# Kernel optimization log

Measured on AMD Instinct MI355X. Metric: run time of the kernel, lower is better.

## Reference

```python
import jax, jax.numpy as jnp
import numpy as np

GAMMA = 0.96875


def setup_inputs() -> dict:
    key = jax.random.key(0)
    kx, kq, kk, kv = jax.random.split(key, 4)
    B, T, D = 4, 2048, 1024
    x = jax.random.normal(kx, (B, T, D), dtype=jnp.float32)
    Wq = jax.random.normal(kq, (D, D), dtype=jnp.float32) * (1.0 / np.sqrt(D))
    Wk = jax.random.normal(kk, (D, D), dtype=jnp.float32) * (1.0 / np.sqrt(D))
    Wv = jax.random.normal(kv, (D, D), dtype=jnp.float32) * (1.0 / np.sqrt(D))
    return {"x": x, "Wq": Wq, "Wk": Wk, "Wv": Wv}


def reference(x, Wq, Wk, Wv):
    # x: [B, T, D_in]; projections are bias-free Dense layers
    B, T, _ = x.shape
    D = Wq.shape[1]
    Q = jnp.einsum("bti,id->btd", x, Wq)  # [B,T,D]
    K = jnp.einsum("bti,id->btd", x, Wk)
    V = jnp.einsum("bti,id->btd", x, Wv)

    gamma = jnp.asarray(GAMMA, x.dtype)

    # Original: s[t] = gamma*s[t-1] + K[:,t,:]^T @ V[:,t,:]   (a [D,D] state,
    # batch is CONTRACTED by the matmul), then only reduce_sum over the last
    # state axis is used. The recurrence is linear, so it collapses exactly to
    # a [D]-vector recurrence with m_t[d] = sum_b K[b,t,d] * (sum_e V[b,t,e]).
    m = jnp.einsum("btd,bt->td", K, V.sum(axis=-1))  # [T,D]

    def step(s, mt):
        s_new = gamma * s + mt
        return s_new, s_new

    # loop runs t = 1..T-1 starting from s = 0; afterwards s[0] = s[1]
    _, states = jax.lax.scan(step, jnp.zeros((D,), x.dtype), m[1:])  # [T-1,D]
    S = jnp.concatenate([states[:1], states], axis=0)  # [T,D]

    # tf.reshape([T,D] -> [-1, T]) is a row-major element scramble, then transpose
    S = S.reshape(-1, T).T  # [T,D] (scrambled, faithful to the original)

    return S[None, :, :] * Q  # broadcast over batch -> [B,T,D]
```

## Files before the change

kernel.cpp:

```cpp
#include <hip/hip_runtime.h>
#include <hip/hip_bf16.h>
#include <cstddef>

#define T_DIM 2048
#define D_DIM 1024
#define GAMMA_F 0.96875f

typedef __attribute__((ext_vector_type(8))) short bf16x8;
typedef __attribute__((ext_vector_type(8))) ushort ushortx8;
typedef __attribute__((ext_vector_type(4))) float f32x4;

#define AS1 __attribute__((address_space(1)))
#define AS3 __attribute__((address_space(3)))

static __device__ inline ushort f2bs(float f) {
    __hip_bfloat16 h = __float2bfloat16(f);
    return *reinterpret_cast<ushort*>(&h);
}

template <int N>
static __device__ __forceinline__ void vm_wait() {
    if constexpr (N == 0)      asm volatile("s_waitcnt vmcnt(0)" ::: "memory");
    else if constexpr (N == 4) asm volatile("s_waitcnt vmcnt(4)" ::: "memory");
    else if constexpr (N == 8) asm volatile("s_waitcnt vmcnt(8)" ::: "memory");
    else                       static_assert(N == 0 || N == 4 || N == 8, "vmcnt");
}
static __device__ __forceinline__ void raw_barrier() {
    asm volatile("s_barrier" ::: "memory");
}

__global__ __launch_bounds__(256) void k_prep(const float* __restrict__ Wk,
                                              const float* __restrict__ Wq,
                                              const float* __restrict__ Wv,
                                              ushort* __restrict__ WTk,
                                              ushort* __restrict__ WTq,
                                              float* __restrict__ wv_sum) {
    const int tid = threadIdx.x;
    if (blockIdx.z == 2) {
        __shared__ float red[4];
        const int i = blockIdx.y * 32 + blockIdx.x;
        const float* row = Wv + (size_t)i * D_DIM;
        float p = 0.f;
        for (int c = tid; c < D_DIM; c += 256) p += row[c];
        for (int o = 32; o; o >>= 1) p += __shfl_down(p, o);
        if ((tid & 63) == 0) red[tid >> 6] = p;
        __syncthreads();
        if (tid == 0) wv_sum[i] = red[0] + red[1] + red[2] + red[3];
        return;
    }
    const float* W = (blockIdx.z == 0) ? Wk : Wq;
    ushort* WT     = (blockIdx.z == 0) ? WTk : WTq;
    __shared__ float tile[32][33];
    const int tx = tid & 31, ty = tid >> 5;
    const int kb = blockIdx.x * 32, nb = blockIdx.y * 32;
    #pragma unroll
    for (int r = 0; r < 4; ++r)
        tile[ty + 8 * r][tx] = W[(size_t)(kb + ty + 8 * r) * 1024 + nb + tx];
    __syncthreads();
    #pragma unroll
    for (int r = 0; r < 4; ++r)
        WT[(size_t)(nb + ty + 8 * r) * 1024 + kb + tx] =
            f2bs(tile[tx][ty + 8 * r]);
}

__global__ __launch_bounds__(256) void k_vsum_y(const float* __restrict__ x,
                                                const float* __restrict__ wv_sum,
                                                ushort* __restrict__ yb,
                                                ushort* __restrict__ xb) {
    __shared__ float xs[4][D_DIM];
    __shared__ float red[4][4];
    const int t = blockIdx.x;
    const int tid = threadIdx.x;
    const int lane = tid & 63, wv = tid >> 6;

    #pragma unroll
    for (int b = 0; b < 4; ++b) {
        const float4* xr = (const float4*)(x + ((size_t)b * T_DIM + t) * D_DIM);
        *(float4*)&xs[b][tid * 4] = xr[tid];
    }
    __syncthreads();

    #pragma unroll
    for (int b = 0; b < 4; ++b) {
        float p = 0.f;
        for (int c = tid; c < D_DIM; c += 256) p += xs[b][c] * wv_sum[c];
        for (int o = 32; o; o >>= 1) p += __shfl_down(p, o);
        if (lane == 0) red[wv][b] = p;
    }
    __syncthreads();

    float vs[4];
    #pragma unroll
    for (int b = 0; b < 4; ++b)
        vs[b] = red[0][b] + red[1][b] + red[2][b] + red[3][b];

    if (tid < 128) {
        const int i0 = tid * 8;
        ushortx8 yv;
        #pragma unroll
        for (int j = 0; j < 8; ++j) {
            float a = 0.f;
            #pragma unroll
            for (int b = 0; b < 4; ++b) a += xs[b][i0 + j] * vs[b];
            yv[j] = f2bs(a);
        }
        *(ushortx8*)(yb + (size_t)t * D_DIM + i0) = yv;
    }
    for (int g = tid; g < 512; g += 256) {
        const int b = g >> 7, i0 = (g & 127) * 8;
        ushortx8 xv;
        #pragma unroll
        for (int j = 0; j < 8; ++j) xv[j] = f2bs(xs[b][i0 + j]);
        *(ushortx8*)(xb + ((size_t)b * T_DIM + t) * D_DIM + i0) = xv;
    }
}

template <int MF, int NF, int EPI>
__global__ __launch_bounds__(256) void k_gemm(const ushort* __restrict__ A,
                                              const ushort* __restrict__ BT,
                                              float* __restrict__ C,
                                              const float* __restrict__ S) {
    constexpr int BM = MF * 32;
    constexpr int BN = NF * 32;
    constexpr int LOADS = BM / 32 + BN / 32;
    __shared__ ushort As[2][BM][64];
    __shared__ ushort Bs[2][BN][64];
    const int tid = threadIdx.x;
    const int lane = tid & 63, wid = tid >> 6;
    const int wr = wid >> 1, wc = wid & 1;
    const int rowBase = blockIdx.x * BM;
    const int colBase = blockIdx.y * BN;

    f32x4 acc[MF][NF];
    #pragma unroll
    for (int i = 0; i < MF; ++i)
        #pragma unroll
        for (int j = 0; j < NF; ++j) acc[i][j] = f32x4{0.f, 0.f, 0.f, 0.f};

    auto stage = [&](int buf, int kb) {
        #pragma unroll
        for (int q = 0; q < BM / 32; ++q) {
            const int s = q * 4096 + tid * 16;
            const int r = s >> 7, grp = (s >> 4) & 7;
            const int gcol = kb + (((grp ^ (r & 7)) & 7) << 3);
            __builtin_amdgcn_global_load_lds(
                (const AS1 void*)(A + (size_t)(rowBase + r) * 1024 + gcol),
                (AS3 void*)((AS3 char*)&As[buf][0][0] + s), 16, 0, 0);
        }
        #pragma unroll
        for (int q = 0; q < BN / 32; ++q) {
            const int s = q * 4096 + tid * 16;
            const int r = s >> 7, grp = (s >> 4) & 7;
            const int gcol = kb + (((grp ^ (r & 7)) & 7) << 3);
            __builtin_amdgcn_global_load_lds(
                (const AS1 void*)(BT + (size_t)(colBase + r) * 1024 + gcol),
                (AS3 void*)((AS3 char*)&Bs[buf][0][0] + s), 16, 0, 0);
        }
    };

    stage(0, 0);

    #pragma unroll 2
    for (int kt = 0; kt < 16; ++kt) {
        const int cur = kt & 1;
        if (kt < 15) {
            stage(cur ^ 1, (kt + 1) * 64);
            vm_wait<LOADS>();
        } else {
            vm_wait<0>();
        }
        raw_barrier();

        bf16x8 af[2][MF], bfv[2][NF];
        #pragma unroll
        for (int ks = 0; ks < 2; ++ks) {
            const int kg = ks * 4 + (lane >> 4);
            #pragma unroll
            for (int mi = 0; mi < MF; ++mi) {
                const int r = wr * (MF * 16) + mi * 16 + (lane & 15);
                af[ks][mi] = *(const bf16x8*)((const char*)&As[cur][0][0] +
                                              r * 128 + (((kg ^ (r & 7)) & 7) << 4));
            }
            #pragma unroll
            for (int ni = 0; ni < NF; ++ni) {
                const int r = wc * (NF * 16) + ni * 16 + (lane & 15);
                bfv[ks][ni] = *(const bf16x8*)((const char*)&Bs[cur][0][0] +
                                               r * 128 + (((kg ^ (r & 7)) & 7) << 4));
            }
        }
        #pragma unroll
        for (int ks = 0; ks < 2; ++ks)
            #pragma unroll
            for (int mi = 0; mi < MF; ++mi)
                #pragma unroll
                for (int ni = 0; ni < NF; ++ni)
                    acc[mi][ni] = __builtin_amdgcn_mfma_f32_16x16x32_bf16(
                        af[ks][mi], bfv[ks][ni], acc[mi][ni], 0, 0, 0);

        asm volatile("s_waitcnt lgkmcnt(0)" ::: "memory");
        raw_barrier();
    }

    #pragma unroll
    for (int mi = 0; mi < MF; ++mi) {
        #pragma unroll
        for (int ni = 0; ni < NF; ++ni) {
            const int col = colBase + wc * (NF * 16) + ni * 16 + (lane & 15);
            #pragma unroll
            for (int q = 0; q < 4; ++q) {
                const int row = rowBase + wr * (MF * 16) + mi * 16 + (lane >> 4) * 4 + q;
                float v = acc[mi][ni][q];
                if (EPI) {
                    const int t = row & (T_DIM - 1);
                    v *= S[(size_t)(2 * col + (t >> 10)) * D_DIM + (t & 1023)];
                }
                C[(size_t)row * D_DIM + col] = v;
            }
        }
    }
}

#define SC_L 32
#define SC_NC 64

__global__ __launch_bounds__(256) void k_scan1(const float* __restrict__ m,
                                               float* __restrict__ tot) {
    const int col = blockIdx.x * 64 + (threadIdx.x & 63);
    const int ch  = blockIdx.y * 4 + (threadIdx.x >> 6);
    const int t0 = ch * SC_L;
    float r = 0.f;
    #pragma unroll 4
    for (int k = 0; k < SC_L; ++k) {
        const int t = t0 + k;
        const float a = (t == 0) ? 0.f : m[(size_t)t * D_DIM + col];
        r = GAMMA_F * r + a;
    }
    tot[(size_t)ch * D_DIM + col] = r;
}

__global__ __launch_bounds__(256) void k_scan2(float* __restrict__ m,
                                               const float* __restrict__ tot) {
    const int col = blockIdx.x * 64 + (threadIdx.x & 63);
    const int ch  = blockIdx.y * 4 + (threadIdx.x >> 6);
    const int t0 = ch * SC_L;

    float gL = 1.f;
    #pragma unroll
    for (int i = 0; i < SC_L; ++i) gL *= GAMMA_F;

    float carry = 0.f, f = 1.f;
    for (int j = ch - 1; j >= 0; --j) {
        carry += f * tot[(size_t)j * D_DIM + col];
        f *= gL;
    }

    float r = carry, s1 = 0.f;
    #pragma unroll 4
    for (int k = 0; k < SC_L; ++k) {
        const int t = t0 + k;
        const float a = (t == 0) ? 0.f : m[(size_t)t * D_DIM + col];
        r = GAMMA_F * r + a;
        m[(size_t)t * D_DIM + col] = r;
        if (t == 1) s1 = r;
    }
    if (ch == 0) m[col] = s1;
}

extern "C" void kernel_launch(void* const* d_in, const int* in_sizes, int n_in,
                              void* d_out, int out_size, void* d_ws, size_t ws_size,
                              hipStream_t stream) {
    const float* x  = (const float*)d_in[0];
    const float* Wq = (const float*)d_in[1];
    const float* Wk = (const float*)d_in[2];
    const float* Wv = (const float*)d_in[3];
    float* out = (float*)d_out;
    char* ws = (char*)d_ws;

    ushort* xb  = (ushort*)(ws);
    float*  m   = (float*)(ws + (16u << 20));
    ushort* yb  = (ushort*)(ws + (24u << 20));
    ushort* WTk = (ushort*)(ws + (28u << 20));
    ushort* WTq = (ushort*)(ws + (30u << 20));
    float*  wv_sum = m;
    float*  tot = (float*)yb;

    dim3 gP(32, 32, 3);
    k_prep<<<gP, 256, 0, stream>>>(Wk, Wq, Wv, WTk, WTq, wv_sum);

    k_vsum_y<<<T_DIM, 256, 0, stream>>>(x, wv_sum, (ushort*)yb, (ushort*)xb);

    dim3 gm(T_DIM / 64, D_DIM / 64);
    k_gemm<2, 2, 0><<<gm, 256, 0, stream>>>(yb, WTk, m, nullptr);

    dim3 gs(D_DIM / 64, SC_NC / 4);
    k_scan1<<<gs, 256, 0, stream>>>(m, tot);
    k_scan2<<<gs, 256, 0, stream>>>(m, tot);

    dim3 gq((4 * T_DIM) / 128, D_DIM / 128);
    k_gemm<4, 4, 1><<<gq, 256, 0, stream>>>(xb, WTq, out, m);
}
```

Before: 90.08 us.

## Pre-scramble scan state into GEMM-friendly layout and move GEMMs to 512-thread blocks

The scan's second pass now writes the scrambled state S through a shared-memory transpose into a separate buffer laid out as [t][col]. The output GEMM epilogue can then read it with coalesced accesses instead of the strided gather it used before. Both GEMMs are also reshaped to 512-thread blocks with 8 waves (4x2), which changes tile sizes and load counts per stage and adds new vmcnt wait variants. The cost is an extra 8MB workspace buffer, and the hidden wave-indexing code must match the new 8-wave layout.

```diff
diff --git a/kernel.cpp b/kernel.cpp
--- a/kernel.cpp
+++ b/kernel.cpp
@@ -21,9 +21,12 @@
 template <int N>
 static __device__ __forceinline__ void vm_wait() {
     if constexpr (N == 0)      asm volatile("s_waitcnt vmcnt(0)" ::: "memory");
+    else if constexpr (N == 2) asm volatile("s_waitcnt vmcnt(2)" ::: "memory");
+    else if constexpr (N == 3) asm volatile("s_waitcnt vmcnt(3)" ::: "memory");
     else if constexpr (N == 4) asm volatile("s_waitcnt vmcnt(4)" ::: "memory");
+    else if constexpr (N == 6) asm volatile("s_waitcnt vmcnt(6)" ::: "memory");
     else if constexpr (N == 8) asm volatile("s_waitcnt vmcnt(8)" ::: "memory");
-    else                       static_assert(N == 0 || N == 4 || N == 8, "vmcnt");
+    else static_assert(N <= 8, "vmcnt");
 }
 static __device__ __forceinline__ void raw_barrier() {
     asm volatile("s_barrier" ::: "memory");
@@ -116,13 +119,13 @@
 }
 
 template <int MF, int NF, int EPI>
-__global__ __launch_bounds__(256) void k_gemm(const ushort* __restrict__ A,
-                                              const ushort* __restrict__ BT,
-                                              float* __restrict__ C,
-                                              const float* __restrict__ S) {
-    constexpr int BM = MF * 32;
-    constexpr int BN = NF * 32;
-    constexpr int LOADS = BM / 32 + BN / 32;
+__global__ __launch_bounds__(512, 4) void k_gemm(const ushort* __restrict__ A,
+                                                 const ushort* __restrict__ BT,
+                                                 float* __restrict__ C,
+                                                 const float* __restrict__ S2) {
+    constexpr int BM = 4 * MF * 16;
+    constexpr int BN = 2 * NF * 16;
+    constexpr int LOADS = BM / 64 + BN / 64;
     __shared__ ushort As[2][BM][64];
     __shared__ ushort Bs[2][BN][64];
     const int tid = threadIdx.x;
@@ -139,8 +142,8 @@
 
     auto stage = [&](int buf, int kb) {
         #pragma unroll
-        for (int q = 0; q < BM / 32; ++q) {
-            const int s = q * 4096 + tid * 16;
+        for (int q = 0; q < BM / 64; ++q) {
+            const int s = q * 8192 + tid * 16;
             const int r = s >> 7, grp = (s >> 4) & 7;
             const int gcol = kb + (((grp ^ (r & 7)) & 7) << 3);
             __builtin_amdgcn_global_load_lds(
@@ -148,8 +151,8 @@
                 (AS3 void*)((AS3 char*)&As[buf][0][0] + s), 16, 0, 0);
         }
         #pragma unroll
-        for (int q = 0; q < BN / 32; ++q) {
-            const int s = q * 4096 + tid * 16;
+        for (int q = 0; q < BN / 64; ++q) {
+            const int s = q * 8192 + tid * 16;
             const int r = s >> 7, grp = (s >> 4) & 7;
             const int gcol = kb + (((grp ^ (r & 7)) & 7) << 3);
             __builtin_amdgcn_global_load_lds(
@@ -210,10 +213,8 @@
             for (int q = 0; q < 4; ++q) {
                 const int row = rowBase + wr * (MF * 16) + mi * 16 + (lane >> 4) * 4 + q;
                 float v = acc[mi][ni][q];
-                if (EPI) {
-                    const int t = row & (T_DIM - 1);
-                    v *= S[(size_t)(2 * col + (t >> 10)) * D_DIM + (t & 1023)];
-                }
+                if (EPI)
+                    v *= S2[(size_t)(row & (T_DIM - 1)) * D_DIM + col];
                 C[(size_t)row * D_DIM + col] = v;
             }
         }
@@ -238,18 +239,23 @@
     tot[(size_t)ch * D_DIM + col] = r;
 }
 
-__global__ __launch_bounds__(256) void k_scan2(float* __restrict__ m,
-                                               const float* __restrict__ tot) {
-    const int col = blockIdx.x * 64 + (threadIdx.x & 63);
-    const int ch  = blockIdx.y * 4 + (threadIdx.x >> 6);
-    const int t0 = ch * SC_L;
+__global__ __launch_bounds__(256) void k_scan2(const float* __restrict__ m,
+                                               const float* __restrict__ tot,
+                                               float* __restrict__ S2) {
+    __shared__ float ls[128][65];
+    const int tid = threadIdx.x;
+    const int cl = tid & 63;
+    const int ch = tid >> 6;
+    const int col = blockIdx.x * 64 + cl;
+    const int chg = blockIdx.y * 4 + ch;
+    const int t0 = chg * SC_L;
 
     float gL = 1.f;
     #pragma unroll
     for (int i = 0; i < SC_L; ++i) gL *= GAMMA_F;
 
     float carry = 0.f, f = 1.f;
-    for (int j = ch - 1; j >= 0; --j) {
+    for (int j = chg - 1; j >= 0; --j) {
         carry += f * tot[(size_t)j * D_DIM + col];
         f *= gL;
     }
@@ -260,10 +266,21 @@
         const int t = t0 + k;
         const float a = (t == 0) ? 0.f : m[(size_t)t * D_DIM + col];
         r = GAMMA_F * r + a;
-        m[(size_t)t * D_DIM + col] = r;
+        ls[ch * SC_L + k][cl] = r;
         if (t == 1) s1 = r;
     }
-    if (ch == 0) m[col] = s1;
+    if (blockIdx.y == 0 && ch == 0) ls[0][cl] = s1;
+    __syncthreads();
+
+    const int c0 = blockIdx.x * 64;
+    const int tB = blockIdx.y * 128;
+    for (int e = tid; e < 128 * 64; e += 256) {
+        const int rr = e >> 6;
+        const int j  = e & 63;
+        const int hi = rr >> 6, cl2 = rr & 63;
+        S2[(size_t)((hi << 10) + c0 + cl2) * D_DIM + (tB >> 1) + j] =
+            ls[2 * j + hi][cl2];
+    }
 }
 
 extern "C" void kernel_launch(void* const* d_in, const int* in_sizes, int n_in,
@@ -281,6 +298,7 @@
     ushort* yb  = (ushort*)(ws + (24u << 20));
     ushort* WTk = (ushort*)(ws + (28u << 20));
     ushort* WTq = (ushort*)(ws + (30u << 20));
+    float*  S2  = (float*)(ws + (32u << 20));
     float*  wv_sum = m;
     float*  tot = (float*)yb;
 
@@ -289,13 +307,13 @@
 
     k_vsum_y<<<T_DIM, 256, 0, stream>>>(x, wv_sum, (ushort*)yb, (ushort*)xb);
 
-    dim3 gm(T_DIM / 64, D_DIM / 64);
-    k_gemm<2, 2, 0><<<gm, 256, 0, stream>>>(yb, WTk, m, nullptr);
+    dim3 gm(T_DIM / 128, D_DIM / 64);
+    k_gemm<2, 2, 0><<<gm, 512, 0, stream>>>(yb, WTk, m, nullptr);
 
     dim3 gs(D_DIM / 64, SC_NC / 4);
     k_scan1<<<gs, 256, 0, stream>>>(m, tot);
-    k_scan2<<<gs, 256, 0, stream>>>(m, tot);
+    k_scan2<<<gs, 256, 0, stream>>>(m, tot, S2);
 
     dim3 gq((4 * T_DIM) / 128, D_DIM / 128);
-    k_gemm<4, 4, 1><<<gq, 256, 0, stream>>>(xb, WTq, out, m);
-}
+    k_gemm<2, 4, 1><<<gq, 512, 0, stream>>>(xb, WTq, out, S2);
+}
```

Result: faster. 80.32 us (-10.8%).
